# Kernel optimization log

Hardware: AMD Instinct MI355X
Metric: run time of the kernel (lower is better)

Reference implementation:

```python
import jax, jax.numpy as jnp
import numpy as np

N = 100_000      # nodes
E = 1_600_000    # edges (avg degree 16)
C_IN = 128
HID = 128        # 2 * out_channels
OUT = 64
EDIM = 1
NEG_SLOPE = 0.2  # PyG GATConv default negative_slope


def _gat(x, src, dst, n, W, a_s, a_d, b, edge_attr=None, We=None, a_e=None):
    """PyG GATConv with heads=1, concat=True, add_self_loops=True (fill_value='mean').
    x: [n, Cin]; src/dst: [E] (messages flow src -> dst); returns [n, Cout].
    """
    xl = x @ W                 # [n, Cout] transformed node features
    a_src = xl @ a_s           # [n] per-node source attention logit
    a_dst = xl @ a_d           # [n] per-node destination attention logit
    loop = jnp.arange(n)
    if edge_attr is not None:
        # self-loop edge_attr = mean of incoming edge_attr per node (fill_value='mean')
        ones = jnp.ones((src.shape[0],), xl.dtype)
        cnt = jax.ops.segment_sum(ones, dst, num_segments=n)              # [n]
        s = jax.ops.segment_sum(edge_attr, dst, num_segments=n)           # [n, EDIM]
        loop_attr = jnp.where(cnt[:, None] > 0, s / jnp.maximum(cnt, 1.0)[:, None], 0.0)
        ea = jnp.concatenate([edge_attr, loop_attr], axis=0)              # [E+n, EDIM]
    src2 = jnp.concatenate([src, loop])
    dst2 = jnp.concatenate([dst, loop])
    alpha = a_src[src2] + a_dst[dst2]                                      # [E+n]
    if edge_attr is not None:
        alpha = alpha + (ea @ We) @ a_e                                    # edge-attribute attention term
    alpha = jax.nn.leaky_relu(alpha, NEG_SLOPE)
    # softmax over incoming edges of each destination node (stable)
    m = jax.ops.segment_max(alpha, dst2, num_segments=n)
    ex = jnp.exp(alpha - m[dst2])
    den = jax.ops.segment_sum(ex, dst2, num_segments=n)
    coef = ex / den[dst2]                                                  # [E+n]
    out = jax.ops.segment_sum(coef[:, None] * xl[src2], dst2, num_segments=n)
    return out + b


def setup_inputs() -> dict:
    key = jax.random.key(0)
    ks = jax.random.split(key, 32)
    s = 0.1
    inp = {
        "x": jax.random.normal(ks[0], (N, C_IN), jnp.float32),
        "edge_index": jax.random.randint(ks[1], (2, E), 0, N, jnp.int64),
        "edge_weights": jax.random.uniform(ks[2], (E, EDIM), jnp.float32),
    }
    def lin(k, i, o):
        return jax.random.normal(k, (i, o), jnp.float32) * s
    def vec(k, c):
        return jax.random.normal(k, (c,), jnp.float32) * s
    # layer 0: 128 -> 128 (with edge attention)
    inp["W0"], inp["as0"], inp["ad0"] = lin(ks[3], C_IN, HID), vec(ks[4], HID), vec(ks[5], HID)
    inp["ae0"], inp["We0"], inp["b0"] = vec(ks[6], HID), lin(ks[7], EDIM, HID), jnp.zeros((HID,), jnp.float32)
    # layer 1: 128 -> 128 (with edge attention)
    inp["W1"], inp["as1"], inp["ad1"] = lin(ks[8], HID, HID), vec(ks[9], HID), vec(ks[10], HID)
    inp["ae1"], inp["We1"], inp["b1"] = vec(ks[11], HID), lin(ks[12], EDIM, HID), jnp.zeros((HID,), jnp.float32)
    # conv_mu: 128 -> 64 (with edge attention)
    inp["Wm"], inp["asm"], inp["adm"] = lin(ks[13], HID, OUT), vec(ks[14], OUT), vec(ks[15], OUT)
    inp["aem"], inp["Wem"], inp["bm"] = vec(ks[16], OUT), lin(ks[17], EDIM, OUT), jnp.zeros((OUT,), jnp.float32)
    # conv_logstd: 128 -> 64 (called WITHOUT edge_attr -> no edge term)
    inp["Wl"], inp["asl"], inp["adl"] = lin(ks[18], HID, OUT), vec(ks[19], OUT), vec(ks[20], OUT)
    inp["bl"] = jnp.zeros((OUT,), jnp.float32)
    return inp


def reference(x, edge_index, edge_weights,
              W0, as0, ad0, ae0, We0, b0,
              W1, as1, ad1, ae1, We1, b1,
              Wm, asm, adm, aem, Wem, bm,
              Wl, asl, adl, bl):
    src, dst = edge_index[0], edge_index[1]
    h = jax.nn.relu(_gat(x, src, dst, N, W0, as0, ad0, b0, edge_weights, We0, ae0))
    h = jax.nn.relu(_gat(h, src, dst, N, W1, as1, ad1, b1, edge_weights, We1, ae1))
    mu = _gat(h, src, dst, N, Wm, asm, adm, bm, edge_weights, Wem, aem)
    logstd = _gat(h, src, dst, N, Wl, asl, adl, bl)  # no edge_attr, per original forward
    return mu, logstd
```

## Files before the change

kernel.cpp:

```cpp
#include <hip/hip_runtime.h>

#define NN 100000
#define EE 1600000

typedef __attribute__((ext_vector_type(8))) __bf16 bf16x8;
typedef __attribute__((ext_vector_type(4))) float f32x4;
typedef unsigned short u16;

__device__ __forceinline__ float bf2f(u16 v) {
  union { unsigned u; float f; } x; x.u = ((unsigned)v) << 16; return x.f;
}
__device__ __forceinline__ u16 f2bf(float f) {
  union { unsigned u; float f; } x; x.f = f;
  x.u += 0x7fffu + ((x.u >> 16) & 1u);
  return (u16)(x.u >> 16);
}
__device__ __forceinline__ float lo_f(unsigned u) {
  union { unsigned u; float f; } x; x.u = u << 16; return x.f;
}
__device__ __forceinline__ float hi_f(unsigned u) {
  union { unsigned u; float f; } x; x.u = u & 0xffff0000u; return x.f;
}
__device__ __forceinline__ float lrelu(float x) { return x > 0.f ? x : 0.2f * x; }
__device__ __forceinline__ int clampi(int v, int hi) {
  return ((unsigned)v < (unsigned)hi) ? v : 0;
}
__device__ __forceinline__ float ldf(const void* p, size_t i, int fl) {
  return fl ? ((const float*)p)[i] : bf2f(((const u16*)p)[i]);
}

__global__ void k_fillf(float* __restrict__ o, int n, float v) {
  int i = blockIdx.x * 256 + threadIdx.x;
  if (i < n) o[i] = v;
}

__global__ void k_zero(int* __restrict__ p, int n) {
  int i = blockIdx.x * 256 + threadIdx.x;
  if (i < n) p[i] = 0;
}

__global__ void k_fdetect(const u16* __restrict__ xb, int* __restrict__ fflag) {
  if (blockIdx.x == 0 && threadIdx.x == 0) {
    int huge = 0;
    for (int i = 0; i < 256; ++i) {
      float v = bf2f(xb[i]);
      float a = fabsf(v);
      if (!(a == a) || a > 1e6f) huge++;
    }
    *fflag = (huge > 0) ? 1 : 0;
  }
}

__global__ void k_detect(const int* __restrict__ ei, int* __restrict__ mode) {
  if (blockIdx.x == 0 && threadIdx.x == 0) {
    int nz = 0;
    for (int j = 1; j < 64; j += 2) nz += (ei[j] != 0);
    *mode = (nz == 0) ? 1 : 0;
  }
}

struct CvtDesc { const void* src; u16* dst; int n; };
struct CvtPack { CvtDesc d[12]; };
__global__ void k_cvt_small(CvtPack p, const int* __restrict__ fflag) {
  int b = blockIdx.x;
  int fl = *fflag;
  const void* src = p.d[b].src;
  u16* dst = p.d[b].dst;
  int n = p.d[b].n;
  for (int i = threadIdx.x; i < n; i += 64)
    dst[i] = fl ? f2bf(((const float*)src)[i]) : ((const u16*)src)[i];
}

__global__ void k_rank(const int* __restrict__ ei, const int* __restrict__ mode,
                       int* __restrict__ cnt, int* __restrict__ rank, int E_) {
  int e = blockIdx.x * 256 + threadIdx.x;
  if (e >= E_) return;
  int m_ = *mode;
  int d = m_ ? ei[2 * (size_t)(E_ + e)] : ei[E_ + e];
  d = clampi(d, NN);
  rank[e] = atomicAdd(&cnt[d], 1);
}

__global__ void k_bsum(const int* __restrict__ cnt, int* __restrict__ bsum, int n) {
  int b = blockIdx.x, t = threadIdx.x;
  int i0 = b * 1024 + t * 4;
  int s = 0;
#pragma unroll
  for (int j = 0; j < 4; ++j) { int i = i0 + j; if (i < n) s += cnt[i]; }
  for (int off = 32; off; off >>= 1) s += __shfl_xor(s, off);
  __shared__ int wt[4];
  int lane = t & 63, w = t >> 6;
  if (lane == 0) wt[w] = s;
  __syncthreads();
  if (t == 0) bsum[b] = wt[0] + wt[1] + wt[2] + wt[3];
}

__global__ void k_scanb(const int* __restrict__ bsum, int* __restrict__ boff, int nchunks) {
  int t = threadIdx.x;
  int lane = t & 63, w = t >> 6;
  int v = (t < nchunks) ? bsum[t] : 0;
  int sc = v;
  for (int off = 1; off < 64; off <<= 1) { int o = __shfl_up(sc, off); if (lane >= off) sc += o; }
  __shared__ int w0tot;
  if (w == 0 && lane == 63) w0tot = sc;
  __syncthreads();
  int incl = sc + (w ? w0tot : 0);
  if (t < nchunks) boff[t] = incl - v;
}

__global__ void k_scan_chunk(const int* __restrict__ cnt, const int* __restrict__ boff,
                             int* __restrict__ row_off, int n, int etot) {
  int b = blockIdx.x, t = threadIdx.x;
  int i0 = b * 1024 + t * 4;
  int v[4]; int s = 0;
#pragma unroll
  for (int j = 0; j < 4; ++j) { int i = i0 + j; v[j] = (i < n) ? cnt[i] : 0; s += v[j]; }
  int lane = t & 63, w = t >> 6;
  int sc = s;
  for (int off = 1; off < 64; off <<= 1) { int o = __shfl_up(sc, off); if (lane >= off) sc += o; }
  __shared__ int wt[4];
  if (lane == 63) wt[w] = sc;
  __syncthreads();
  int woff = 0;
  for (int k = 0; k < w; ++k) woff += wt[k];
  int ex = boff[b] + woff + sc - s;
#pragma unroll
  for (int j = 0; j < 4; ++j) { int i = i0 + j; if (i < n) row_off[i] = ex; ex += v[j]; }
  if (b == 0 && t == 0) row_off[n] = etot;
}

__global__ void k_place(const int* __restrict__ ei, const int* __restrict__ mode,
                        const void* __restrict__ ew, const int* __restrict__ fflag,
                        const int* __restrict__ row_off, const int* __restrict__ rank,
                        int* __restrict__ esrc, u16* __restrict__ eww, int E_) {
  int e = blockIdx.x * 256 + threadIdx.x;
  if (e >= E_) return;
  int m_ = *mode;
  int s = m_ ? ei[2 * (size_t)e] : ei[e];
  int d = m_ ? ei[2 * (size_t)(E_ + e)] : ei[E_ + e];
  s = clampi(s, NN);
  d = clampi(d, NN);
  int p = row_off[d] + rank[e];
  if (p >= 0 && p < E_) {
    esrc[p] = s;
    eww[p] = f2bf(ldf(ew, e, *fflag));
  }
}

__global__ void k_loop2(const int* __restrict__ row_off, const u16* __restrict__ eww,
                        float* __restrict__ la, int n) {
  int i = blockIdx.x * 256 + threadIdx.x;
  if (i >= n) return;
  int b = row_off[i], e = row_off[i + 1];
  float s = 0.f;
  for (int j = b; j < e; ++j) s += bf2f(eww[j]);
  la[i] = (e > b) ? s / (float)(e - b) : 0.f;
}

__global__ void k_tr(const void* __restrict__ W, const int* __restrict__ fflag,
                     u16* __restrict__ WT, int M) {
  int i = blockIdx.x * 256 + threadIdx.x;
  if (i >= 128 * M) return;
  int k = i / M, m = i % M;
  WT[m * 128 + k] = f2bf(ldf(W, i, *fflag));
}

__global__ void k_dots(const void* We0, const void* ae0, const void* We1, const void* ae1,
                       const void* Wem, const void* aem, const int* __restrict__ fflag,
                       float* c) {
  int b = blockIdx.x;
  const void *w_, *a_; int m;
  if (b == 0)      { w_ = We0; a_ = ae0; m = 128; }
  else if (b == 1) { w_ = We1; a_ = ae1; m = 128; }
  else             { w_ = Wem; a_ = aem; m = 64; }
  int lane = threadIdx.x;
  int fl = *fflag;
  float s = 0.f;
  for (int j = lane; j < m; j += 64) s += ldf(w_, j, fl) * ldf(a_, j, fl);
  for (int off = 32; off; off >>= 1) s += __shfl_xor(s, off);
  if (lane == 0) { c[b] = s; if (b == 0) c[3] = 0.f; }
}

template<bool FLEXA, bool DUAL>
__global__ __launch_bounds__(256) void k_gemm(
    const void* __restrict__ Araw, const int* __restrict__ fflag,
    const u16* __restrict__ WT,
    const u16* __restrict__ avs, const u16* __restrict__ avd,
    u16* __restrict__ xl,
    float* __restrict__ asrcA, float* __restrict__ adstA,
    float* __restrict__ asrcB, float* __restrict__ adstB, int n) {
  const int K = 128;
  int lane = threadIdx.x & 63;
  int wave = threadIdx.x >> 6;
  int quad = lane >> 4;
  int l16 = lane & 15;
  int r0 = (blockIdx.x * 4 + wave) * 16;
  if (r0 >= n) return;
  int arow = r0 + l16; if (arow >= n) arow = n - 1;
  bf16x8 afr[4];
  int fl = FLEXA ? fflag[0] : 0;
  if (FLEXA && fl) {
    const float* af = (const float*)Araw + (size_t)arow * K + quad * 8;
#pragma unroll
    for (int kb = 0; kb < 4; ++kb) {
      float4 f0 = *(const float4*)(af + kb * 32);
      float4 f1 = *(const float4*)(af + kb * 32 + 4);
      union { bf16x8 v; u16 s[8]; } t;
      t.s[0] = f2bf(f0.x); t.s[1] = f2bf(f0.y); t.s[2] = f2bf(f0.z); t.s[3] = f2bf(f0.w);
      t.s[4] = f2bf(f1.x); t.s[5] = f2bf(f1.y); t.s[6] = f2bf(f1.z); t.s[7] = f2bf(f1.w);
      afr[kb] = t.v;
    }
  } else {
    const u16* ab = (const u16*)Araw + (size_t)arow * K + quad * 8;
#pragma unroll
    for (int kb = 0; kb < 4; ++kb) afr[kb] = *(const bf16x8*)(ab + kb * 32);
  }
  f32x4 acc[8];
#pragma unroll
  for (int nb = 0; nb < 8; ++nb) acc[nb] = (f32x4){0.f, 0.f, 0.f, 0.f};
#pragma unroll
  for (int nb = 0; nb < 8; ++nb) {
    const u16* bbase = WT + (size_t)(nb * 16 + l16) * K + quad * 8;
#pragma unroll
    for (int kb = 0; kb < 4; ++kb) {
      bf16x8 bfr = *(const bf16x8*)(bbase + kb * 32);
      acc[nb] = __builtin_amdgcn_mfma_f32_16x16x32_bf16(afr[kb], bfr, acc[nb], 0, 0, 0);
    }
  }
  float ps[2][4] = {{0,0,0,0},{0,0,0,0}}, pd[2][4] = {{0,0,0,0},{0,0,0,0}};
#pragma unroll
  for (int nb = 0; nb < 8; ++nb) {
    const int g = (DUAL && nb >= 4) ? 1 : 0;
    int col = nb * 16 + l16;
    float vs = bf2f(avs[col]), vd = bf2f(avd[col]);
#pragma unroll
    for (int r = 0; r < 4; ++r) {
      int row = r0 + quad * 4 + r;
      float v = acc[nb][r];
      if (row < n) xl[(size_t)row * 128 + col] = f2bf(v);
      ps[g][r] += v * vs;
      pd[g][r] += v * vd;
    }
  }
#pragma unroll
  for (int off = 1; off < 16; off <<= 1) {
#pragma unroll
    for (int r = 0; r < 4; ++r) {
      ps[0][r] += __shfl_xor(ps[0][r], off);
      pd[0][r] += __shfl_xor(pd[0][r], off);
      if (DUAL) {
        ps[1][r] += __shfl_xor(ps[1][r], off);
        pd[1][r] += __shfl_xor(pd[1][r], off);
      }
    }
  }
  if (l16 == 0) {
#pragma unroll
    for (int r = 0; r < 4; ++r) {
      int row = r0 + quad * 4 + r;
      if (row < n) {
        asrcA[row] = ps[0][r]; adstA[row] = pd[0][r];
        if (DUAL) { asrcB[row] = ps[1][r]; adstB[row] = pd[1][r]; }
      }
    }
  }
}

__global__ __launch_bounds__(256) void k_agg(
    const int* __restrict__ row_off, const int* __restrict__ esrc,
    const u16* __restrict__ eww,
    const float* __restrict__ asrc, const float* __restrict__ adst,
    const float* __restrict__ la, const float* __restrict__ cptr,
    const u16* __restrict__ xl, const u16* __restrict__ bias,
    u16* __restrict__ out, int n) {
  __shared__ float lp[4][64];
  __shared__ int lsv[4][64];
  int wid = (blockIdx.x * blockDim.x + threadIdx.x) >> 6;
  if (wid >= n) return;
  int w = threadIdx.x >> 6;
  int d = __builtin_amdgcn_readfirstlane(wid);
  int lane = threadIdx.x & 63;
  float c = cptr[0];
  float ad = adst[d];
  float aL = lrelu(asrc[d] + ad + c * la[d]);
  float m = aL, den = 1.f;
  unsigned su = *(const unsigned*)(xl + (size_t)d * 128 + 2 * lane);
  float A0 = lo_f(su), A1 = hi_f(su);
  int beg = row_off[d], end = row_off[d + 1];
  for (int base = beg; base < end; base += 64) {
    int i = base + lane;
    bool v = i < end;
    int s = v ? esrc[i] : 0;
    float al = v ? lrelu(asrc[s] + ad + c * bf2f(eww[i])) : -3e38f;
    float cm = al;
#pragma unroll
    for (int off = 32; off; off >>= 1) cm = fmaxf(cm, __shfl_xor(cm, off));
    if (cm > m) {
      float f = __expf(m - cm);
      A0 *= f; A1 *= f; den *= f;
      m = cm;
    }
    float e = v ? __expf(al - m) : 0.f;
    lp[w][lane] = e; lsv[w][lane] = s;
    float es = e;
#pragma unroll
    for (int off = 32; off; off >>= 1) es += __shfl_xor(es, off);
    den += es;
    int cnt = end - base; if (cnt > 64) cnt = 64;
    float B0 = 0.f, B1 = 0.f, C0 = 0.f, C1 = 0.f, D0 = 0.f, D1 = 0.f;
    int j = 0;
    for (; j + 4 <= cnt; j += 4) {
      float p0 = lp[w][j + 0]; int s0 = lsv[w][j + 0];
      float p1 = lp[w][j + 1]; int s1 = lsv[w][j + 1];
      float p2 = lp[w][j + 2]; int s2 = lsv[w][j + 2];
      float p3 = lp[w][j + 3]; int s3 = lsv[w][j + 3];
      unsigned u0 = *(const unsigned*)(xl + (size_t)s0 * 128 + 2 * lane);
      unsigned u1 = *(const unsigned*)(xl + (size_t)s1 * 128 + 2 * lane);
      unsigned u2 = *(const unsigned*)(xl + (size_t)s2 * 128 + 2 * lane);
      unsigned u3 = *(const unsigned*)(xl + (size_t)s3 * 128 + 2 * lane);
      A0 = fmaf(p0, lo_f(u0), A0); A1 = fmaf(p0, hi_f(u0), A1);
      B0 = fmaf(p1, lo_f(u1), B0); B1 = fmaf(p1, hi_f(u1), B1);
      C0 = fmaf(p2, lo_f(u2), C0); C1 = fmaf(p2, hi_f(u2), C1);
      D0 = fmaf(p3, lo_f(u3), D0); D1 = fmaf(p3, hi_f(u3), D1);
    }
    for (; j < cnt; ++j) {
      float p0 = lp[w][j]; int s0 = lsv[w][j];
      unsigned u0 = *(const unsigned*)(xl + (size_t)s0 * 128 + 2 * lane);
      A0 = fmaf(p0, lo_f(u0), A0); A1 = fmaf(p0, hi_f(u0), A1);
    }
    A0 += B0 + C0 + D0; A1 += B1 + C1 + D1;
  }
  float inv = 1.f / den;
  float o0 = fmaxf(fmaf(A0, inv, bf2f(bias[2 * lane])), 0.f);
  float o1 = fmaxf(fmaf(A1, inv, bf2f(bias[2 * lane + 1])), 0.f);
  unsigned uo = (unsigned)f2bf(o0) | ((unsigned)f2bf(o1) << 16);
  *(unsigned*)(out + (size_t)d * 128 + 2 * lane) = uo;
}

__global__ __launch_bounds__(256) void k_aggh(
    const int* __restrict__ row_off, const int* __restrict__ esrc,
    const u16* __restrict__ eww,
    const float* __restrict__ asA, const float* __restrict__ adA,
    const float* __restrict__ asB, const float* __restrict__ adB,
    const float* __restrict__ la, const float* __restrict__ cptr,
    const u16* __restrict__ xl, const u16* __restrict__ bias,
    float* __restrict__ outf, int n) {
  __shared__ float lpA[4][64];
  __shared__ float lpB[4][64];
  __shared__ int lsv[4][64];
  int wid = (blockIdx.x * blockDim.x + threadIdx.x) >> 6;
  if (wid >= n) return;
  int w = threadIdx.x >> 6;
  int d = __builtin_amdgcn_readfirstlane(wid);
  int lane = threadIdx.x & 63;
  bool isMu = lane < 32;
  float c = cptr[0];
  float adAd = adA[d], adBd = adB[d];
  float aLA = lrelu(asA[d] + adAd + c * la[d]);
  float aLB = lrelu(asB[d] + adBd);
  float mA = aLA, mB = aLB, denA = 1.f, denB = 1.f;
  unsigned su = *(const unsigned*)(xl + (size_t)d * 128 + 2 * lane);
  float A0 = lo_f(su), A1 = hi_f(su);
  int beg = row_off[d], end = row_off[d + 1];
  for (int base = beg; base < end; base += 64) {
    int i = base + lane;
    bool v = i < end;
    int s = v ? esrc[i] : 0;
    float sa = v ? asA[s] : 0.f, sb = v ? asB[s] : 0.f;
    float alA = v ? lrelu(sa + adAd + c * bf2f(eww[i])) : -3e38f;
    float alB = v ? lrelu(sb + adBd) : -3e38f;
    float cmA = alA, cmB = alB;
#pragma unroll
    for (int off = 32; off; off >>= 1) {
      cmA = fmaxf(cmA, __shfl_xor(cmA, off));
      cmB = fmaxf(cmB, __shfl_xor(cmB, off));
    }
    float fA = 1.f, fB = 1.f;
    if (cmA > mA) { fA = __expf(mA - cmA); mA = cmA; denA *= fA; }
    if (cmB > mB) { fB = __expf(mB - cmB); mB = cmB; denB *= fB; }
    float f = isMu ? fA : fB;
    A0 *= f; A1 *= f;
    float eA = v ? __expf(alA - mA) : 0.f;
    float eB = v ? __expf(alB - mB) : 0.f;
    lpA[w][lane] = eA; lpB[w][lane] = eB; lsv[w][lane] = s;
    float esA = eA, esB = eB;
#pragma unroll
    for (int off = 32; off; off >>= 1) {
      esA += __shfl_xor(esA, off);
      esB += __shfl_xor(esB, off);
    }
    denA += esA; denB += esB;
    const float* lpp = isMu ? lpA[w] : lpB[w];
    int cnt = end - base; if (cnt > 64) cnt = 64;
    float B0 = 0.f, B1 = 0.f, C0 = 0.f, C1 = 0.f, D0 = 0.f, D1 = 0.f;
    int j = 0;
    for (; j + 4 <= cnt; j += 4) {
      float p0 = lpp[j + 0]; int s0 = lsv[w][j + 0];
      float p1 = lpp[j + 1]; int s1 = lsv[w][j + 1];
      float p2 = lpp[j + 2]; int s2 = lsv[w][j + 2];
      float p3 = lpp[j + 3]; int s3 = lsv[w][j + 3];
      unsigned u0 = *(const unsigned*)(xl + (size_t)s0 * 128 + 2 * lane);
      unsigned u1 = *(const unsigned*)(xl + (size_t)s1 * 128 + 2 * lane);
      unsigned u2 = *(const unsigned*)(xl + (size_t)s2 * 128 + 2 * lane);
      unsigned u3 = *(const unsigned*)(xl + (size_t)s3 * 128 + 2 * lane);
      A0 = fmaf(p0, lo_f(u0), A0); A1 = fmaf(p0, hi_f(u0), A1);
      B0 = fmaf(p1, lo_f(u1), B0); B1 = fmaf(p1, hi_f(u1), B1);
      C0 = fmaf(p2, lo_f(u2), C0); C1 = fmaf(p2, hi_f(u2), C1);
      D0 = fmaf(p3, lo_f(u3), D0); D1 = fmaf(p3, hi_f(u3), D1);
    }
    for (; j < cnt; ++j) {
      float p0 = lpp[j]; int s0 = lsv[w][j];
      unsigned u0 = *(const unsigned*)(xl + (size_t)s0 * 128 + 2 * lane);
      A0 = fmaf(p0, lo_f(u0), A0); A1 = fmaf(p0, hi_f(u0), A1);
    }
    A0 += B0 + C0 + D0; A1 += B1 + C1 + D1;
  }
  float inv = isMu ? (1.f / denA) : (1.f / denB);
  int col0 = 2 * lane;
  float o0 = fmaf(A0, inv, bf2f(bias[col0]));
  float o1 = fmaf(A1, inv, bf2f(bias[col0 + 1]));
  float* ob = isMu ? (outf + (size_t)d * 64 + col0)
                   : (outf + (size_t)NN * 64 + (size_t)d * 64 + (col0 - 64));
  ob[0] = o0; ob[1] = o1;
}

extern "C" void kernel_launch(void* const* d_in, const int* in_sizes, int n_in,
                              void* d_out, int out_size, void* d_ws, size_t ws_size,
                              hipStream_t stream) {
  (void)in_sizes; (void)n_in;
  const int* ei = (const int*)d_in[1];
  float* outf = (float*)d_out;

  u16* regionA = (u16*)d_out;
  u16* regionB = (u16*)d_out + (size_t)NN * 128;

  char* p = (char*)d_ws;
  auto alloc = [&](size_t bytes) -> char* {
    char* r = p; p += (bytes + 255) & ~(size_t)255; return r;
  };
  char* z0      = p;
  int*   cnt    = (int*)alloc(NN * 4);
  size_t zbytes = (size_t)(p - z0);
  int*   row_off= (int*)alloc((NN + 1) * 4);
  int*   bsum   = (int*)alloc(512);
  int*   boff   = (int*)alloc(512);
  int*   mode   = (int*)alloc(256);
  int*   fflag  = (int*)alloc(256);
  float* la     = (float*)alloc(NN * 4);
  float* asrcA  = (float*)alloc(NN * 4);
  float* adstA  = (float*)alloc(NN * 4);
  float* asrcB  = (float*)alloc(NN * 4);
  float* adstB  = (float*)alloc(NN * 4);
  int*   esrc   = (int*)alloc((size_t)EE * 4);
  u16*   eww    = (u16*)alloc((size_t)EE * 2);
  u16*   WT0    = (u16*)alloc(128 * 128 * 2);
  u16*   WT1    = (u16*)alloc(128 * 128 * 2);
  u16*   WTh    = (u16*)alloc(128 * 128 * 2);
  float* cvals  = (float*)alloc(16);
  u16*   vecc   = (u16*)alloc(9 * 256);
  u16*   xl     = (u16*)alloc((size_t)NN * 128 * 2);

  int* rank = (int*)xl;

  size_t NEED = (size_t)(p - (char*)d_ws);
  if (ws_size < NEED) {
    k_fillf<<<(out_size + 255) / 256, 256, 0, stream>>>(outf, out_size, 0.125f);
    return;
  }

  u16* as0c = vecc + 0 * 128; u16* ad0c = vecc + 1 * 128; u16* b0c = vecc + 2 * 128;
  u16* as1c = vecc + 3 * 128; u16* ad1c = vecc + 4 * 128; u16* b1c = vecc + 5 * 128;
  u16* hvs  = vecc + 6 * 128; u16* hvd  = vecc + 7 * 128; u16* bh  = vecc + 8 * 128;

  k_fdetect<<<1, 64, 0, stream>>>((const u16*)d_in[0], fflag);
  k_detect<<<1, 64, 0, stream>>>(ei, mode);

  CvtPack pk;
  pk.d[0]  = {d_in[4],  as0c, 128};
  pk.d[1]  = {d_in[5],  ad0c, 128};
  pk.d[2]  = {d_in[8],  b0c,  128};
  pk.d[3]  = {d_in[10], as1c, 128};
  pk.d[4]  = {d_in[11], ad1c, 128};
  pk.d[5]  = {d_in[14], b1c,  128};
  pk.d[6]  = {d_in[16], hvs,      64};
  pk.d[7]  = {d_in[22], hvs + 64, 64};
  pk.d[8]  = {d_in[17], hvd,      64};
  pk.d[9]  = {d_in[23], hvd + 64, 64};
  pk.d[10] = {d_in[20], bh,       64};
  pk.d[11] = {d_in[24], bh + 64,  64};
  k_cvt_small<<<12, 64, 0, stream>>>(pk, fflag);

  const int nz = (int)(zbytes / 4);
  k_zero<<<(nz + 255) / 256, 256, 0, stream>>>((int*)z0, nz);

  const int Eblocks = (EE + 255) / 256;
  const int nchunks = (NN + 1023) / 1024;
  k_rank<<<Eblocks, 256, 0, stream>>>(ei, mode, cnt, rank, EE);
  k_bsum<<<nchunks, 256, 0, stream>>>(cnt, bsum, NN);
  k_scanb<<<1, 128, 0, stream>>>(bsum, boff, nchunks);
  k_scan_chunk<<<nchunks, 256, 0, stream>>>(cnt, boff, row_off, NN, EE);
  k_place<<<Eblocks, 256, 0, stream>>>(ei, mode, d_in[2], fflag, row_off, rank, esrc, eww, EE);
  k_loop2<<<(NN + 255) / 256, 256, 0, stream>>>(row_off, eww, la, NN);
  k_tr<<<64, 256, 0, stream>>>(d_in[3],  fflag, WT0, 128);
  k_tr<<<64, 256, 0, stream>>>(d_in[9],  fflag, WT1, 128);
  k_tr<<<32, 256, 0, stream>>>(d_in[15], fflag, WTh, 64);
  k_tr<<<32, 256, 0, stream>>>(d_in[21], fflag, WTh + 64 * 128, 64);
  k_dots<<<3, 64, 0, stream>>>(d_in[7], d_in[6], d_in[13], d_in[12], d_in[19], d_in[18],
                               fflag, cvals);

  const int gblocks = (((NN + 15) / 16) + 3) / 4;
  const int eblocks = (int)(((size_t)NN * 64 + 255) / 256);

  k_gemm<true, false><<<gblocks, 256, 0, stream>>>(d_in[0], fflag, WT0, as0c, ad0c,
                                                   xl, asrcA, adstA, nullptr, nullptr, NN);
  k_agg<<<eblocks, 256, 0, stream>>>(row_off, esrc, eww, asrcA, adstA, la,
                                     cvals + 0, xl, b0c, regionB, NN);
  k_gemm<false, false><<<gblocks, 256, 0, stream>>>(regionB, fflag, WT1, as1c, ad1c,
                                                    xl, asrcA, adstA, nullptr, nullptr, NN);
  k_agg<<<eblocks, 256, 0, stream>>>(row_off, esrc, eww, asrcA, adstA, la,
                                     cvals + 1, xl, b1c, regionA, NN);
  k_gemm<false, true><<<gblocks, 256, 0, stream>>>(regionA, fflag, WTh, hvs, hvd,
                                                   xl, asrcA, adstA, asrcB, adstB, NN);
  k_aggh<<<eblocks, 256, 0, stream>>>(row_off, esrc, eww, asrcA, adstA, asrcB, adstB,
                                      la, cvals + 2, xl, bh, outf, NN);
}
```

Baseline: 617.8 us.

## Fuse setup kernels, overlap rank with first GEMM, pack edges, drop online max

Merges the zeroing, flag detection, small-vector conversion, weight transposes and dot products into one k_setup launch. Flags are now recomputed per wave with ballots instead of stored. The edge-rank atomics share a launch with the layer-0 GEMM, with rank moved into the output buffer. Edge source and weight are packed into one int2 array, and the two source logits are packed into a float2. The aggregation kernels drop the online-softmax running max and per-chunk shuffle reductions and shift by the self-loop logit instead. This cuts launch count and per-edge work, but exp can overflow if an edge logit greatly exceeds the self-loop logit.

```diff
diff --git a/kernel.cpp b/kernel.cpp
--- a/kernel.cpp
+++ b/kernel.cpp
@@ -29,56 +29,75 @@
   return fl ? ((const float*)p)[i] : bf2f(((const u16*)p)[i]);
 }
 
+__device__ __forceinline__ int wave_fdetect(const u16* __restrict__ xb) {
+  int lane = threadIdx.x & 63;
+  int bad = 0;
+#pragma unroll
+  for (int j = 0; j < 4; ++j) {
+    float a = fabsf(bf2f(xb[lane * 4 + j]));
+    bad |= (!(a == a) || a > 1e6f) ? 1 : 0;
+  }
+  return (__ballot(bad) != 0ull) ? 1 : 0;
+}
+__device__ __forceinline__ int wave_mdetect(const int* __restrict__ ei) {
+  int lane = threadIdx.x & 63;
+  int v = (lane < 32) ? ei[2 * lane + 1] : 0;
+  return (__ballot(v != 0) == 0ull) ? 1 : 0;
+}
+
 __global__ void k_fillf(float* __restrict__ o, int n, float v) {
   int i = blockIdx.x * 256 + threadIdx.x;
   if (i < n) o[i] = v;
 }
 
-__global__ void k_zero(int* __restrict__ p, int n) {
-  int i = blockIdx.x * 256 + threadIdx.x;
-  if (i < n) p[i] = 0;
-}
-
-__global__ void k_fdetect(const u16* __restrict__ xb, int* __restrict__ fflag) {
-  if (blockIdx.x == 0 && threadIdx.x == 0) {
-    int huge = 0;
-    for (int i = 0; i < 256; ++i) {
-      float v = bf2f(xb[i]);
-      float a = fabsf(v);
-      if (!(a == a) || a > 1e6f) huge++;
-    }
-    *fflag = (huge > 0) ? 1 : 0;
-  }
-}
-
-__global__ void k_detect(const int* __restrict__ ei, int* __restrict__ mode) {
-  if (blockIdx.x == 0 && threadIdx.x == 0) {
-    int nz = 0;
-    for (int j = 1; j < 64; j += 2) nz += (ei[j] != 0);
-    *mode = (nz == 0) ? 1 : 0;
-  }
-}
-
 struct CvtDesc { const void* src; u16* dst; int n; };
-struct CvtPack { CvtDesc d[12]; };
-__global__ void k_cvt_small(CvtPack p, const int* __restrict__ fflag) {
-  int b = blockIdx.x;
-  int fl = *fflag;
-  const void* src = p.d[b].src;
-  u16* dst = p.d[b].dst;
-  int n = p.d[b].n;
-  for (int i = threadIdx.x; i < n; i += 64)
-    dst[i] = fl ? f2bf(((const float*)src)[i]) : ((const u16*)src)[i];
-}
-
-__global__ void k_rank(const int* __restrict__ ei, const int* __restrict__ mode,
-                       int* __restrict__ cnt, int* __restrict__ rank, int E_) {
-  int e = blockIdx.x * 256 + threadIdx.x;
-  if (e >= E_) return;
-  int m_ = *mode;
-  int d = m_ ? ei[2 * (size_t)(E_ + e)] : ei[E_ + e];
-  d = clampi(d, NN);
-  rank[e] = atomicAdd(&cnt[d], 1);
+struct SetupArgs {
+  CvtDesc cvt[12];
+  const void* W[4]; u16* WT[4]; int WM[4];
+  const void* dw[3]; const void* da[3]; int dm[3];
+  float* cvals;
+  int* cnt;
+  const u16* xb;
+};
+__global__ __launch_bounds__(256) void k_setup(SetupArgs a) {
+  int b = blockIdx.x, t = threadIdx.x;
+  const int ZB = (NN + 255) / 256;
+  if (b < ZB) { int i = b * 256 + t; if (i < NN) a.cnt[i] = 0; return; }
+  b -= ZB;
+  if (b < 12) {
+    int fl = wave_fdetect(a.xb);
+    const void* src = a.cvt[b].src; u16* dst = a.cvt[b].dst; int n = a.cvt[b].n;
+    for (int i = t; i < n; i += 256)
+      dst[i] = fl ? f2bf(((const float*)src)[i]) : ((const u16*)src)[i];
+    return;
+  }
+  b -= 12;
+  if (b < 192) {
+    int fl = wave_fdetect(a.xb);
+    int wsel, lb;
+    if (b < 64)       { wsel = 0; lb = b; }
+    else if (b < 128) { wsel = 1; lb = b - 64; }
+    else if (b < 160) { wsel = 2; lb = b - 128; }
+    else              { wsel = 3; lb = b - 160; }
+    int M = a.WM[wsel];
+    int i = lb * 256 + t;
+    if (i < 128 * M) {
+      int k = i / M, m = i % M;
+      a.WT[wsel][m * 128 + k] = f2bf(ldf(a.W[wsel], i, fl));
+    }
+    return;
+  }
+  b -= 192;
+  if (b < 3) {
+    if (t < 64) {
+      int fl = wave_fdetect(a.xb);
+      float s = 0.f; int m = a.dm[b];
+      for (int j = t; j < m; j += 64) s += ldf(a.dw[b], j, fl) * ldf(a.da[b], j, fl);
+      for (int off = 32; off; off >>= 1) s += __shfl_xor(s, off);
+      if (t == 0) a.cvals[b] = s;
+    }
+    return;
+  }
 }
 
 __global__ void k_bsum(const int* __restrict__ cnt, int* __restrict__ bsum, int n) {
@@ -129,77 +148,24 @@
   if (b == 0 && t == 0) row_off[n] = etot;
 }
 
-__global__ void k_place(const int* __restrict__ ei, const int* __restrict__ mode,
-                        const void* __restrict__ ew, const int* __restrict__ fflag,
-                        const int* __restrict__ row_off, const int* __restrict__ rank,
-                        int* __restrict__ esrc, u16* __restrict__ eww, int E_) {
-  int e = blockIdx.x * 256 + threadIdx.x;
-  if (e >= E_) return;
-  int m_ = *mode;
-  int s = m_ ? ei[2 * (size_t)e] : ei[e];
-  int d = m_ ? ei[2 * (size_t)(E_ + e)] : ei[E_ + e];
-  s = clampi(s, NN);
-  d = clampi(d, NN);
-  int p = row_off[d] + rank[e];
-  if (p >= 0 && p < E_) {
-    esrc[p] = s;
-    eww[p] = f2bf(ldf(ew, e, *fflag));
-  }
-}
-
-__global__ void k_loop2(const int* __restrict__ row_off, const u16* __restrict__ eww,
-                        float* __restrict__ la, int n) {
-  int i = blockIdx.x * 256 + threadIdx.x;
-  if (i >= n) return;
-  int b = row_off[i], e = row_off[i + 1];
-  float s = 0.f;
-  for (int j = b; j < e; ++j) s += bf2f(eww[j]);
-  la[i] = (e > b) ? s / (float)(e - b) : 0.f;
-}
-
-__global__ void k_tr(const void* __restrict__ W, const int* __restrict__ fflag,
-                     u16* __restrict__ WT, int M) {
-  int i = blockIdx.x * 256 + threadIdx.x;
-  if (i >= 128 * M) return;
-  int k = i / M, m = i % M;
-  WT[m * 128 + k] = f2bf(ldf(W, i, *fflag));
-}
-
-__global__ void k_dots(const void* We0, const void* ae0, const void* We1, const void* ae1,
-                       const void* Wem, const void* aem, const int* __restrict__ fflag,
-                       float* c) {
-  int b = blockIdx.x;
-  const void *w_, *a_; int m;
-  if (b == 0)      { w_ = We0; a_ = ae0; m = 128; }
-  else if (b == 1) { w_ = We1; a_ = ae1; m = 128; }
-  else             { w_ = Wem; a_ = aem; m = 64; }
-  int lane = threadIdx.x;
-  int fl = *fflag;
-  float s = 0.f;
-  for (int j = lane; j < m; j += 64) s += ldf(w_, j, fl) * ldf(a_, j, fl);
-  for (int off = 32; off; off >>= 1) s += __shfl_xor(s, off);
-  if (lane == 0) { c[b] = s; if (b == 0) c[3] = 0.f; }
-}
-
-template<bool FLEXA, bool DUAL>
-__global__ __launch_bounds__(256) void k_gemm(
-    const void* __restrict__ Araw, const int* __restrict__ fflag,
+template<bool DUAL>
+__device__ __forceinline__ void gemm_body(
+    int bid, int fl, const void* __restrict__ Araw,
     const u16* __restrict__ WT,
     const u16* __restrict__ avs, const u16* __restrict__ avd,
     u16* __restrict__ xl,
-    float* __restrict__ asrcA, float* __restrict__ adstA,
-    float* __restrict__ asrcB, float* __restrict__ adstB, int n) {
+    float* __restrict__ asrc, float* __restrict__ adst,
+    float2* __restrict__ asAB, float* __restrict__ adstB, int n) {
   const int K = 128;
   int lane = threadIdx.x & 63;
   int wave = threadIdx.x >> 6;
   int quad = lane >> 4;
   int l16 = lane & 15;
-  int r0 = (blockIdx.x * 4 + wave) * 16;
+  int r0 = (bid * 4 + wave) * 16;
   if (r0 >= n) return;
   int arow = r0 + l16; if (arow >= n) arow = n - 1;
   bf16x8 afr[4];
-  int fl = FLEXA ? fflag[0] : 0;
-  if (FLEXA && fl) {
+  if (fl) {
     const float* af = (const float*)Araw + (size_t)arow * K + quad * 8;
 #pragma unroll
     for (int kb = 0; kb < 4; ++kb) {
@@ -259,16 +225,74 @@
     for (int r = 0; r < 4; ++r) {
       int row = r0 + quad * 4 + r;
       if (row < n) {
-        asrcA[row] = ps[0][r]; adstA[row] = pd[0][r];
-        if (DUAL) { asrcB[row] = ps[1][r]; adstB[row] = pd[1][r]; }
+        if (DUAL) {
+          asAB[row] = make_float2(ps[0][r], ps[1][r]);
+          adst[row] = pd[0][r]; adstB[row] = pd[1][r];
+        } else {
+          asrc[row] = ps[0][r]; adst[row] = pd[0][r];
+        }
       }
     }
   }
 }
 
+__global__ __launch_bounds__(256) void k_rkgemm(
+    const int* __restrict__ ei, int* __restrict__ cnt, int* __restrict__ rank,
+    const u16* __restrict__ xb, const void* __restrict__ Araw,
+    const u16* __restrict__ WT, const u16* __restrict__ avs, const u16* __restrict__ avd,
+    u16* __restrict__ xl, float* __restrict__ asrc, float* __restrict__ adst,
+    int n, int gemmBlocks) {
+  if ((int)blockIdx.x < gemmBlocks) {
+    int fl = wave_fdetect(xb);
+    gemm_body<false>(blockIdx.x, fl, Araw, WT, avs, avd, xl, asrc, adst,
+                     nullptr, nullptr, n);
+  } else {
+    int m_ = wave_mdetect(ei);
+    int e = ((int)blockIdx.x - gemmBlocks) * 256 + threadIdx.x;
+    if (e >= EE) return;
+    int d = m_ ? ei[2 * (size_t)(EE + e)] : ei[EE + e];
+    d = clampi(d, NN);
+    rank[e] = atomicAdd(&cnt[d], 1);
+  }
+}
+
+template<bool DUAL>
+__global__ __launch_bounds__(256) void k_gemm(
+    const u16* __restrict__ A, const u16* __restrict__ WT,
+    const u16* __restrict__ avs, const u16* __restrict__ avd,
+    u16* __restrict__ xl, float* __restrict__ asrc, float* __restrict__ adst,
+    float2* __restrict__ asAB, float* __restrict__ adstB, int n) {
+  gemm_body<DUAL>(blockIdx.x, 0, A, WT, avs, avd, xl, asrc, adst, asAB, adstB, n);
+}
+
+__global__ void k_place(const int* __restrict__ ei, const void* __restrict__ ew,
+                        const u16* __restrict__ xb,
+                        const int* __restrict__ row_off, const int* __restrict__ rank,
+                        int2* __restrict__ edges) {
+  int m_ = wave_mdetect(ei);
+  int fl = wave_fdetect(xb);
+  int e = blockIdx.x * 256 + threadIdx.x;
+  if (e >= EE) return;
+  int s = m_ ? ei[2 * (size_t)e] : ei[e];
+  int d = m_ ? ei[2 * (size_t)(EE + e)] : ei[EE + e];
+  s = clampi(s, NN);
+  d = clampi(d, NN);
+  int p = row_off[d] + rank[e];
+  if (p >= 0 && p < EE) edges[p] = make_int2(s, (int)f2bf(ldf(ew, e, fl)));
+}
+
+__global__ void k_loop2(const int* __restrict__ row_off, const int2* __restrict__ edges,
+                        float* __restrict__ la, int n) {
+  int i = blockIdx.x * 256 + threadIdx.x;
+  if (i >= n) return;
+  int b = row_off[i], e = row_off[i + 1];
+  float s = 0.f;
+  for (int j = b; j < e; ++j) s += bf2f((u16)(edges[j].y & 0xffff));
+  la[i] = (e > b) ? s / (float)(e - b) : 0.f;
+}
+
 __global__ __launch_bounds__(256) void k_agg(
-    const int* __restrict__ row_off, const int* __restrict__ esrc,
-    const u16* __restrict__ eww,
+    const int* __restrict__ row_off, const int2* __restrict__ edges,
     const float* __restrict__ asrc, const float* __restrict__ adst,
     const float* __restrict__ la, const float* __restrict__ cptr,
     const u16* __restrict__ xl, const u16* __restrict__ bias,
@@ -283,29 +307,22 @@
   float c = cptr[0];
   float ad = adst[d];
   float aL = lrelu(asrc[d] + ad + c * la[d]);
-  float m = aL, den = 1.f;
+  float lsum = 0.f;
   unsigned su = *(const unsigned*)(xl + (size_t)d * 128 + 2 * lane);
   float A0 = lo_f(su), A1 = hi_f(su);
   int beg = row_off[d], end = row_off[d + 1];
   for (int base = beg; base < end; base += 64) {
     int i = base + lane;
     bool v = i < end;
-    int s = v ? esrc[i] : 0;
-    float al = v ? lrelu(asrc[s] + ad + c * bf2f(eww[i])) : -3e38f;
-    float cm = al;
-#pragma unroll
-    for (int off = 32; off; off >>= 1) cm = fmaxf(cm, __shfl_xor(cm, off));
-    if (cm > m) {
-      float f = __expf(m - cm);
-      A0 *= f; A1 *= f; den *= f;
-      m = cm;
-    }
-    float e = v ? __expf(al - m) : 0.f;
+    int2 ev = v ? edges[i] : make_int2(0, 0);
+    int s = ev.x;
+    float e = 0.f;
+    if (v) {
+      float al = lrelu(asrc[s] + ad + c * bf2f((u16)(ev.y & 0xffff)));
+      e = __expf(al - aL);
+    }
+    lsum += e;
     lp[w][lane] = e; lsv[w][lane] = s;
-    float es = e;
-#pragma unroll
-    for (int off = 32; off; off >>= 1) es += __shfl_xor(es, off);
-    den += es;
     int cnt = end - base; if (cnt > 64) cnt = 64;
     float B0 = 0.f, B1 = 0.f, C0 = 0.f, C1 = 0.f, D0 = 0.f, D1 = 0.f;
     int j = 0;
@@ -330,7 +347,9 @@
     }
     A0 += B0 + C0 + D0; A1 += B1 + C1 + D1;
   }
-  float inv = 1.f / den;
+#pragma unroll
+  for (int off = 32; off; off >>= 1) lsum += __shfl_xor(lsum, off);
+  float inv = 1.f / (lsum + 1.f);
   float o0 = fmaxf(fmaf(A0, inv, bf2f(bias[2 * lane])), 0.f);
   float o1 = fmaxf(fmaf(A1, inv, bf2f(bias[2 * lane + 1])), 0.f);
   unsigned uo = (unsigned)f2bf(o0) | ((unsigned)f2bf(o1) << 16);
@@ -338,10 +357,9 @@
 }
 
 __global__ __launch_bounds__(256) void k_aggh(
-    const int* __restrict__ row_off, const int* __restrict__ esrc,
-    const u16* __restrict__ eww,
-    const float* __restrict__ asA, const float* __restrict__ adA,
-    const float* __restrict__ asB, const float* __restrict__ adB,
+    const int* __restrict__ row_off, const int2* __restrict__ edges,
+    const float2* __restrict__ asAB, const float* __restrict__ adA,
+    const float* __restrict__ adB,
     const float* __restrict__ la, const float* __restrict__ cptr,
     const u16* __restrict__ xl, const u16* __restrict__ bias,
     float* __restrict__ outf, int n) {
@@ -356,40 +374,26 @@
   bool isMu = lane < 32;
   float c = cptr[0];
   float adAd = adA[d], adBd = adB[d];
-  float aLA = lrelu(asA[d] + adAd + c * la[d]);
-  float aLB = lrelu(asB[d] + adBd);
-  float mA = aLA, mB = aLB, denA = 1.f, denB = 1.f;
+  float2 abd = asAB[d];
+  float aLA = lrelu(abd.x + adAd + c * la[d]);
+  float aLB = lrelu(abd.y + adBd);
+  float lsA = 0.f, lsB = 0.f;
   unsigned su = *(const unsigned*)(xl + (size_t)d * 128 + 2 * lane);
   float A0 = lo_f(su), A1 = hi_f(su);
   int beg = row_off[d], end = row_off[d + 1];
   for (int base = beg; base < end; base += 64) {
     int i = base + lane;
     bool v = i < end;
-    int s = v ? esrc[i] : 0;
-    float sa = v ? asA[s] : 0.f, sb = v ? asB[s] : 0.f;
-    float alA = v ? lrelu(sa + adAd + c * bf2f(eww[i])) : -3e38f;
-    float alB = v ? lrelu(sb + adBd) : -3e38f;
-    float cmA = alA, cmB = alB;
-#pragma unroll
-    for (int off = 32; off; off >>= 1) {
-      cmA = fmaxf(cmA, __shfl_xor(cmA, off));
-      cmB = fmaxf(cmB, __shfl_xor(cmB, off));
-    }
-    float fA = 1.f, fB = 1.f;
-    if (cmA > mA) { fA = __expf(mA - cmA); mA = cmA; denA *= fA; }
-    if (cmB > mB) { fB = __expf(mB - cmB); mB = cmB; denB *= fB; }
-    float f = isMu ? fA : fB;
-    A0 *= f; A1 *= f;
-    float eA = v ? __expf(alA - mA) : 0.f;
-    float eB = v ? __expf(alB - mB) : 0.f;
+    int2 ev = v ? edges[i] : make_int2(0, 0);
+    int s = ev.x;
+    float eA = 0.f, eB = 0.f;
+    if (v) {
+      float2 ab = asAB[s];
+      eA = __expf(lrelu(ab.x + adAd + c * bf2f((u16)(ev.y & 0xffff))) - aLA);
+      eB = __expf(lrelu(ab.y + adBd) - aLB);
+    }
+    lsA += eA; lsB += eB;
     lpA[w][lane] = eA; lpB[w][lane] = eB; lsv[w][lane] = s;
-    float esA = eA, esB = eB;
-#pragma unroll
-    for (int off = 32; off; off >>= 1) {
-      esA += __shfl_xor(esA, off);
-      esB += __shfl_xor(esB, off);
-    }
-    denA += esA; denB += esB;
     const float* lpp = isMu ? lpA[w] : lpB[w];
     int cnt = end - base; if (cnt > 64) cnt = 64;
     float B0 = 0.f, B1 = 0.f, C0 = 0.f, C1 = 0.f, D0 = 0.f, D1 = 0.f;
@@ -415,7 +419,12 @@
     }
     A0 += B0 + C0 + D0; A1 += B1 + C1 + D1;
   }
-  float inv = isMu ? (1.f / denA) : (1.f / denB);
+#pragma unroll
+  for (int off = 32; off; off >>= 1) {
+    lsA += __shfl_xor(lsA, off);
+    lsB += __shfl_xor(lsB, off);
+  }
+  float inv = 1.f / ((isMu ? lsA : lsB) + 1.f);
   int col0 = 2 * lane;
   float o0 = fmaf(A0, inv, bf2f(bias[col0]));
   float o1 = fmaf(A1, inv, bf2f(bias[col0 + 1]));
@@ -429,30 +438,27 @@
                               hipStream_t stream) {
   (void)in_sizes; (void)n_in;
   const int* ei = (const int*)d_in[1];
+  const u16* xb = (const u16*)d_in[0];
   float* outf = (float*)d_out;
 
   u16* regionA = (u16*)d_out;
   u16* regionB = (u16*)d_out + (size_t)NN * 128;
+  int* rank = (int*)d_out;
 
   char* p = (char*)d_ws;
   auto alloc = [&](size_t bytes) -> char* {
     char* r = p; p += (bytes + 255) & ~(size_t)255; return r;
   };
-  char* z0      = p;
   int*   cnt    = (int*)alloc(NN * 4);
-  size_t zbytes = (size_t)(p - z0);
   int*   row_off= (int*)alloc((NN + 1) * 4);
   int*   bsum   = (int*)alloc(512);
   int*   boff   = (int*)alloc(512);
-  int*   mode   = (int*)alloc(256);
-  int*   fflag  = (int*)alloc(256);
   float* la     = (float*)alloc(NN * 4);
   float* asrcA  = (float*)alloc(NN * 4);
   float* adstA  = (float*)alloc(NN * 4);
-  float* asrcB  = (float*)alloc(NN * 4);
   float* adstB  = (float*)alloc(NN * 4);
-  int*   esrc   = (int*)alloc((size_t)EE * 4);
-  u16*   eww    = (u16*)alloc((size_t)EE * 2);
+  float2* asAB  = (float2*)alloc((size_t)NN * 8);
+  int2*  edges  = (int2*)alloc((size_t)EE * 8);
   u16*   WT0    = (u16*)alloc(128 * 128 * 2);
   u16*   WT1    = (u16*)alloc(128 * 128 * 2);
   u16*   WTh    = (u16*)alloc(128 * 128 * 2);
@@ -460,8 +466,6 @@
   u16*   vecc   = (u16*)alloc(9 * 256);
   u16*   xl     = (u16*)alloc((size_t)NN * 128 * 2);
 
-  int* rank = (int*)xl;
-
   size_t NEED = (size_t)(p - (char*)d_ws);
   if (ws_size < NEED) {
     k_fillf<<<(out_size + 255) / 256, 256, 0, stream>>>(outf, out_size, 0.125f);
@@ -472,55 +476,52 @@
   u16* as1c = vecc + 3 * 128; u16* ad1c = vecc + 4 * 128; u16* b1c = vecc + 5 * 128;
   u16* hvs  = vecc + 6 * 128; u16* hvd  = vecc + 7 * 128; u16* bh  = vecc + 8 * 128;
 
-  k_fdetect<<<1, 64, 0, stream>>>((const u16*)d_in[0], fflag);
-  k_detect<<<1, 64, 0, stream>>>(ei, mode);
-
-  CvtPack pk;
-  pk.d[0]  = {d_in[4],  as0c, 128};
-  pk.d[1]  = {d_in[5],  ad0c, 128};
-  pk.d[2]  = {d_in[8],  b0c,  128};
-  pk.d[3]  = {d_in[10], as1c, 128};
-  pk.d[4]  = {d_in[11], ad1c, 128};
-  pk.d[5]  = {d_in[14], b1c,  128};
-  pk.d[6]  = {d_in[16], hvs,      64};
-  pk.d[7]  = {d_in[22], hvs + 64, 64};
-  pk.d[8]  = {d_in[17], hvd,      64};
-  pk.d[9]  = {d_in[23], hvd + 64, 64};
-  pk.d[10] = {d_in[20], bh,       64};
-  pk.d[11] = {d_in[24], bh + 64,  64};
-  k_cvt_small<<<12, 64, 0, stream>>>(pk, fflag);
-
-  const int nz = (int)(zbytes / 4);
-  k_zero<<<(nz + 255) / 256, 256, 0, stream>>>((int*)z0, nz);
+  SetupArgs sa;
+  sa.cvt[0]  = {d_in[4],  as0c, 128};
+  sa.cvt[1]  = {d_in[5],  ad0c, 128};
+  sa.cvt[2]  = {d_in[8],  b0c,  128};
+  sa.cvt[3]  = {d_in[10], as1c, 128};
+  sa.cvt[4]  = {d_in[11], ad1c, 128};
+  sa.cvt[5]  = {d_in[14], b1c,  128};
+  sa.cvt[6]  = {d_in[16], hvs,      64};
+  sa.cvt[7]  = {d_in[22], hvs + 64, 64};
+  sa.cvt[8]  = {d_in[17], hvd,      64};
+  sa.cvt[9]  = {d_in[23], hvd + 64, 64};
+  sa.cvt[10] = {d_in[20], bh,       64};
+  sa.cvt[11] = {d_in[24], bh + 64,  64};
+  sa.W[0] = d_in[3];  sa.WT[0] = WT0;            sa.WM[0] = 128;
+  sa.W[1] = d_in[9];  sa.WT[1] = WT1;            sa.WM[1] = 128;
+  sa.W[2] = d_in[15]; sa.WT[2] = WTh;            sa.WM[2] = 64;
+  sa.W[3] = d_in[21]; sa.WT[3] = WTh + 64 * 128; sa.WM[3] = 64;
+  sa.dw[0] = d_in[7];  sa.da[0] = d_in[6];  sa.dm[0] = 128;
+  sa.dw[1] = d_in[13]; sa.da[1] = d_in[12]; sa.dm[1] = 128;
+  sa.dw[2] = d_in[19]; sa.da[2] = d_in[18]; sa.dm[2] = 64;
+  sa.cvals = cvals; sa.cnt = cnt; sa.xb = xb;
+  const int ZB = (NN + 255) / 256;
+  k_setup<<<ZB + 12 + 192 + 3, 256, 0, stream>>>(sa);
 
   const int Eblocks = (EE + 255) / 256;
   const int nchunks = (NN + 1023) / 1024;
-  k_rank<<<Eblocks, 256, 0, stream>>>(ei, mode, cnt, rank, EE);
+  const int gblocks = (((NN + 15) / 16) + 3) / 4;
+  const int eblocks = (int)(((size_t)NN * 64 + 255) / 256);
+
+  k_rkgemm<<<gblocks + Eblocks, 256, 0, stream>>>(ei, cnt, rank, xb, d_in[0],
+                                                  WT0, as0c, ad0c, xl, asrcA, adstA,
+                                                  NN, gblocks);
   k_bsum<<<nchunks, 256, 0, stream>>>(cnt, bsum, NN);
   k_scanb<<<1, 128, 0, stream>>>(bsum, boff, nchunks);
   k_scan_chunk<<<nchunks, 256, 0, stream>>>(cnt, boff, row_off, NN, EE);
-  k_place<<<Eblocks, 256, 0, stream>>>(ei, mode, d_in[2], fflag, row_off, rank, esrc, eww, EE);
-  k_loop2<<<(NN + 255) / 256, 256, 0, stream>>>(row_off, eww, la, NN);
-  k_tr<<<64, 256, 0, stream>>>(d_in[3],  fflag, WT0, 128);
-  k_tr<<<64, 256, 0, stream>>>(d_in[9],  fflag, WT1, 128);
-  k_tr<<<32, 256, 0, stream>>>(d_in[15], fflag, WTh, 64);
-  k_tr<<<32, 256, 0, stream>>>(d_in[21], fflag, WTh + 64 * 128, 64);
-  k_dots<<<3, 64, 0, stream>>>(d_in[7], d_in[6], d_in[13], d_in[12], d_in[19], d_in[18],
-                               fflag, cvals);
-
-  const int gblocks = (((NN + 15) / 16) + 3) / 4;
-  const int eblocks = (int)(((size_t)NN * 64 + 255) / 256);
-
-  k_gemm<true, false><<<gblocks, 256, 0, stream>>>(d_in[0], fflag, WT0, as0c, ad0c,
-                                                   xl, asrcA, adstA, nullptr, nullptr, NN);
-  k_agg<<<eblocks, 256, 0, stream>>>(row_off, esrc, eww, asrcA, adstA, la,
+  k_place<<<Eblocks, 256, 0, stream>>>(ei, d_in[2], xb, row_off, rank, edges);
+  k_loop2<<<(NN + 255) / 256, 256, 0, stream>>>(row_off, edges, la, NN);
+
+  k_agg<<<eblocks, 256, 0, stream>>>(row_off, edges, asrcA, adstA, la,
                                      cvals + 0, xl, b0c, regionB, NN);
-  k_gemm<false, false><<<gblocks, 256, 0, stream>>>(regionB, fflag, WT1, as1c, ad1c,
-                                                    xl, asrcA, adstA, nullptr, nullptr, NN);
-  k_agg<<<eblocks, 256, 0, stream>>>(row_off, esrc, eww, asrcA, adstA, la,
+  k_gemm<false><<<gblocks, 256, 0, stream>>>(regionB, WT1, as1c, ad1c,
+                                             xl, asrcA, adstA, nullptr, nullptr, NN);
+  k_agg<<<eblocks, 256, 0, stream>>>(row_off, edges, asrcA, adstA, la,
                                      cvals + 1, xl, b1c, regionA, NN);
-  k_gemm<false, true><<<gblocks, 256, 0, stream>>>(regionA, fflag, WTh, hvs, hvd,
-                                                   xl, asrcA, adstA, asrcB, adstB, NN);
-  k_aggh<<<eblocks, 256, 0, stream>>>(row_off, esrc, eww, asrcA, adstA, asrcB, adstB,
+  k_gemm<true><<<gblocks, 256, 0, stream>>>(regionA, WTh, hvs, hvd,
+                                            xl, nullptr, adstA, asAB, adstB, NN);
+  k_aggh<<<eblocks, 256, 0, stream>>>(row_off, edges, asAB, adstA, adstB,
                                       la, cvals + 2, xl, bh, outf, NN);
 }
```

Measured after the change: 565.4 us. 1.09x faster.
